# Kernel optimization log

Measured on AMD Instinct MI355X. Metric: run time of the kernel, lower is better.

Reference implementation:

```python
import jax, jax.numpy as jnp
import numpy as np

TINY = 1e-6

def _norm(x):
    return x / (jnp.linalg.norm(x, axis=-1, keepdims=True) + TINY)

def setup_inputs() -> dict:
    key = jax.random.key(0)
    ks = jax.random.split(key, 8)
    N, L, S, H = 8192, 128, 8, 16
    points = jax.random.normal(ks[0], (N, 3), dtype=jnp.float32)
    normals = _norm(jax.random.normal(ks[1], (N, 3), dtype=jnp.float32))
    # orthonormal root rotation (world -> canonical)
    root_rot, _ = jnp.linalg.qr(jax.random.normal(ks[2], (3, 3), dtype=jnp.float32))
    lgtSGLobes = jax.random.normal(ks[3], (L, 3), dtype=jnp.float32)
    # SG sharpness must be > 1 so arccos(1 - 1/lambda) is well defined
    lgtSGLambdas = jax.random.uniform(ks[4], (L, 1), dtype=jnp.float32) * 30.0 + 5.0
    r_theta_random = jax.random.uniform(ks[5], (N, L, S), dtype=jnp.float32)
    W1 = jax.random.normal(ks[6], (6, H), dtype=jnp.float32) * 0.5
    b1 = jnp.zeros((H,), dtype=jnp.float32)
    W2 = jax.random.normal(ks[7], (H, 1), dtype=jnp.float32) * 0.5
    b2 = jnp.zeros((1,), dtype=jnp.float32)
    return {"points": points, "normals": normals, "root_rot": root_rot,
            "lgtSGLobes": lgtSGLobes, "lgtSGLambdas": lgtSGLambdas,
            "r_theta_random": r_theta_random, "W1": W1, "b1": b1, "W2": W2, "b2": b2}

def reference(points, normals, root_rot, lgtSGLobes, lgtSGLambdas,
              r_theta_random, W1, b1, W2, b2):
    # points/normals: [N,3]; lgtSGLobes: [L,3]; r_theta_random: [N,L,S]
    N = points.shape[0]
    L, S = r_theta_random.shape[1], r_theta_random.shape[2]
    l = _norm(lgtSGLobes)                                  # [L,3] SG lobe axes
    z = jnp.zeros_like(l).at[:, 2].set(1.0)
    U = _norm(jnp.cross(z, l))                             # local frame around lobe
    V = _norm(jnp.cross(l, U))
    sharp = lgtSGLambdas[:, 0]                             # [L]
    r_phi = jnp.clip(jnp.arccos(1.0 - 1.0 / sharp), None, np.pi / 3.0)  # [L]
    lin = (jnp.arange(S, dtype=points.dtype) / S)          # stratified offsets
    r_theta = (r_theta_random / S + lin) * (2.0 * np.pi)   # [N,L,S]
    st, ct = jnp.sin(r_theta), jnp.cos(r_theta)            # [N,L,S]
    sp, cp = jnp.sin(r_phi), jnp.cos(r_phi)                # [L]
    # importance-sampled directions around each lobe: [N,L,S,3]
    sample_dir = (U[None, :, None, :] * (ct * sp[None, :, None])[..., None]
                  + V[None, :, None, :] * (st * sp[None, :, None])[..., None]
                  + l[None, :, None, :] * cp[None, :, None, None])
    # hemisphere mask (normals . sample_dir > eps)
    cos_term = jnp.einsum('nd,nlsd->nls', normals, sample_dir) > TINY
    # rotate query dirs to canonical frame: (-dir) @ root_rot
    input_dir = jnp.einsum('nlsd,de->nlse', -sample_dir, root_rot)
    # visibility MLP on (point, dir); concat avoided by splitting W1
    h = jax.nn.relu(jnp.einsum('nlsd,dh->nlsh', input_dir, W1[3:])
                    + (points @ W1[:3])[:, None, None, :] + b1)   # [N,L,S,H]
    pred_vis = jax.nn.sigmoid(jnp.einsum('nlsh,ho->nlso', h, W2)[..., 0] + b2[0])
    vis = jnp.where(cos_term, pred_vis, 0.0)               # masked scatter-back
    # SG weights exp(lambda*(dir.lobe - 1)); weighted reduction over samples
    w = jnp.exp(sharp[None, :, None] * (jnp.einsum('nlsd,ld->nls', sample_dir, l) - 1.0))
    return jnp.sum(vis * w, axis=-1) / (jnp.sum(w, axis=-1) + TINY)  # [N,L]
```

## Files before the change

kernel.cpp:

```cpp
#include <hip/hip_runtime.h>
#include <math.h>

typedef _Float16 h2 __attribute__((ext_vector_type(2)));
typedef __fp16  hh2 __attribute__((ext_vector_type(2)));

constexpr int Lc = 128;
constexpr int Sc = 8;

constexpr int F_OFF  = 3072;
constexpr int WQ_OFF = 4096;
constexpr int PB_OFF = 4224;
constexpr int LDS_DW = 4240;

static __device__ __forceinline__ h2 pk(float a, float b) {
    return __builtin_bit_cast(h2, __builtin_amdgcn_cvt_pkrtz(a, b));
}
static __device__ __forceinline__ h2 u2h(unsigned u) {
    return __builtin_bit_cast(h2, u);
}
static __device__ __forceinline__ unsigned h2u(h2 v) {
    return __builtin_bit_cast(unsigned, v);
}
static __device__ __forceinline__ float fdot2f(h2 a, h2 b, float c) {
#if __has_builtin(__builtin_amdgcn_fdot2)
    return __builtin_amdgcn_fdot2(__builtin_bit_cast(hh2, a),
                                  __builtin_bit_cast(hh2, b), c, false);
#else
    return c + (float)a.x * (float)b.x + (float)a.y * (float)b.y;
#endif
}
static __device__ __forceinline__ float fast_exp2(float x) {
#if __has_builtin(__builtin_amdgcn_exp2f)
    return __builtin_amdgcn_exp2f(x);
#else
    return exp2f(x);
#endif
}

__global__ __launch_bounds__(256, 4) void vis_fused(
    const float* __restrict__ points,
    const float* __restrict__ normals,
    const float* __restrict__ root_rot,
    const float* __restrict__ lobes,
    const float* __restrict__ lambdas,
    const float* __restrict__ rtheta,
    const float* __restrict__ W1,
    const float* __restrict__ b1,
    const float* __restrict__ W2,
    const float* __restrict__ b2,
    float* __restrict__ out, int N)
{
    __shared__ __align__(16) unsigned lds[LDS_DW];
    const int tid = threadIdx.x;
    const int li  = tid & (Lc - 1);

    {
        float lx = lobes[li*3+0], ly = lobes[li*3+1], lz = lobes[li*3+2];
        float inv = 1.0f / (sqrtf(lx*lx + ly*ly + lz*lz) + 1e-6f);
        lx *= inv; ly *= inv; lz *= inv;

        float ux = -ly, uy = lx;
        inv = 1.0f / (sqrtf(ux*ux + uy*uy) + 1e-6f);
        ux *= inv; uy *= inv;

        float vx = -lz*uy, vy = lz*ux, vz = lx*uy - ly*ux;
        inv = 1.0f / (sqrtf(vx*vx + vy*vy + vz*vz) + 1e-6f);
        vx *= inv; vy *= inv; vz *= inv;

        float sharp = lambdas[li];
        float cp = fmaxf(1.0f - 1.0f/sharp, 0.5f);
        float sp = sqrtf(fmaxf(1.0f - cp*cp, 0.0f));

        float uxs = ux*sp, uys = uy*sp;
        float vxs = vx*sp, vys = vy*sp, vzs = vz*sp;
        float lxc = lx*cp, lyc = ly*cp, lzc = lz*cp;

        const float r0 = root_rot[0], r1 = root_rot[1], r2 = root_rot[2];
        const float r3 = root_rot[3], r4 = root_rot[4], r5 = root_rot[5];
        const float r6 = root_rot[6], r7 = root_rot[7], r8 = root_rot[8];

        float Ur0 = -(uxs*r0 + uys*r3);
        float Ur1 = -(uxs*r1 + uys*r4);
        float Ur2 = -(uxs*r2 + uys*r5);
        float Vr0 = -(vxs*r0 + vys*r3 + vzs*r6);
        float Vr1 = -(vxs*r1 + vys*r4 + vzs*r7);
        float Vr2 = -(vxs*r2 + vys*r5 + vzs*r8);
        float Lr0 = -(lxc*r0 + lyc*r3 + lzc*r6);
        float Lr1 = -(lxc*r1 + lyc*r4 + lzc*r7);
        float Lr2 = -(lxc*r2 + lyc*r5 + lzc*r8);

        const int k0 = (tid < 128) ? 0 : 4;
        unsigned av[4], bv[4], dv[4];
        #pragma unroll
        for (int j = 0; j < 4; ++j) {
            int h0 = 2*(k0 + j), h1 = h0 + 1;
            float a0  = Ur0*W1[48+h0] + Ur1*W1[64+h0] + Ur2*W1[80+h0];
            float a1  = Ur0*W1[48+h1] + Ur1*W1[64+h1] + Ur2*W1[80+h1];
            float bb0 = Vr0*W1[48+h0] + Vr1*W1[64+h0] + Vr2*W1[80+h0];
            float bb1 = Vr0*W1[48+h1] + Vr1*W1[64+h1] + Vr2*W1[80+h1];
            float d0  = Lr0*W1[48+h0] + Lr1*W1[64+h0] + Lr2*W1[80+h0];
            float d1  = Lr0*W1[48+h1] + Lr1*W1[64+h1] + Lr2*W1[80+h1];
            av[j] = h2u(pk(a0, a1));
            bv[j] = h2u(pk(bb0, bb1));
            dv[j] = h2u(pk(d0, d1));
        }
        #pragma unroll
        for (int j = 0; j < 4; j += 2) {
            int g = (k0 + j) >> 1;
            *(uint2*)(lds + (0*4 + g)*256 + li*2) = (uint2){av[j], av[j+1]};
            *(uint2*)(lds + (1*4 + g)*256 + li*2) = (uint2){bv[j], bv[j+1]};
            *(uint2*)(lds + (2*4 + g)*256 + li*2) = (uint2){dv[j], dv[j+1]};
        }

        float* wf = (float*)lds;
        if (tid < 128) {
            *(float2*)(wf + F_OFF + 0*256 + li*2) = (float2){uxs, uys};
            *(float2*)(wf + F_OFF + 1*256 + li*2) = (float2){vxs, vys};
            *(float2*)(wf + F_OFF + 2*256 + li*2) = (float2){vzs, lxc};
            *(float2*)(wf + F_OFF + 3*256 + li*2) = (float2){lyc, lzc};
            float wq = __expf(sharp * (cp - 1.0f));
            wf[WQ_OFF + li] = wq / (8.0f * wq + 1e-6f);
        } else if (tid < 130) {
            int p = (blockIdx.x << 1) + (tid - 128);
            if (p < N) {
                float px = points[3*p], py = points[3*p+1], pz = points[3*p+2];
                #pragma unroll
                for (int k = 0; k < 8; ++k) {
                    int h0 = 2*k, h1 = 2*k + 1;
                    float v0 = b1[h0] + px*W1[h0] + py*W1[16+h0] + pz*W1[32+h0];
                    float v1 = b1[h1] + px*W1[h1] + py*W1[16+h1] + pz*W1[32+h1];
                    lds[PB_OFF + (tid - 128)*8 + k] = h2u(pk(v0, v1));
                }
            }
        }
    }
    __syncthreads();

    const int idx = blockIdx.x * 256 + tid;
    if (idx >= N * Lc) return;
    const int n = (blockIdx.x << 1) + (tid >> 7);

    uint2 t[12];
    #pragma unroll
    for (int g = 0; g < 12; ++g)
        t[g] = *(const uint2*)(lds + g*256 + li*2);
    const float* wf = (const float*)lds;
    float2 g0 = *(const float2*)(wf + F_OFF + 0*256 + li*2);
    float2 g1 = *(const float2*)(wf + F_OFF + 1*256 + li*2);
    float2 g2 = *(const float2*)(wf + F_OFF + 2*256 + li*2);
    float2 g3 = *(const float2*)(wf + F_OFF + 3*256 + li*2);
    float wqp = wf[WQ_OFF + li];

    const float4 q0 = *reinterpret_cast<const float4*>(rtheta + (size_t)idx * Sc);
    const float4 q1 = *reinterpret_cast<const float4*>(rtheta + (size_t)idx * Sc + 4);
    float rs[Sc] = {q0.x, q0.y, q0.z, q0.w, q1.x, q1.y, q1.z, q1.w};

    int nu = __builtin_amdgcn_readfirstlane(n);
    const float* nn = normals + 3*(size_t)nu;
    float nx = nn[0], ny = nn[1], nz = nn[2];
    const unsigned* pbp = lds + PB_OFF + (tid >> 7)*8;

    h2 A[8] = {u2h(t[0].x), u2h(t[0].y), u2h(t[1].x), u2h(t[1].y),
               u2h(t[2].x), u2h(t[2].y), u2h(t[3].x), u2h(t[3].y)};
    h2 B[8] = {u2h(t[4].x), u2h(t[4].y), u2h(t[5].x), u2h(t[5].y),
               u2h(t[6].x), u2h(t[6].y), u2h(t[7].x), u2h(t[7].y)};
    h2 G[8] = {u2h(pbp[0]) + u2h(t[8].x),  u2h(pbp[1]) + u2h(t[8].y),
               u2h(pbp[2]) + u2h(t[9].x),  u2h(pbp[3]) + u2h(t[9].y),
               u2h(pbp[4]) + u2h(t[10].x), u2h(pbp[5]) + u2h(t[10].y),
               u2h(pbp[6]) + u2h(t[11].x), u2h(pbp[7]) + u2h(t[11].y)};

    h2 W2h[8];
    #pragma unroll
    for (int k = 0; k < 8; ++k) W2h[k] = pk(W2[2*k], W2[2*k+1]);
    float b2c = -b2[0] * 1.44269504f;

    float nU = nx*g0.x + ny*g0.y;
    float nV = nx*g1.x + ny*g1.y + nz*g2.x;
    float nL = nx*g2.y + ny*g3.x + nz*g3.y;

    const h2 zero = {(_Float16)0.0f, (_Float16)0.0f};
    float svis = 0.0f;
    #pragma unroll
    for (int s = 0; s < Sc; ++s) {
        float f  = fmaf(rs[s], 0.125f, (float)s * 0.125f);
        float st = __builtin_amdgcn_sinf(f);
        float ct = __builtin_amdgcn_cosf(f);
        float ndot = fmaf(ct, nU, fmaf(st, nV, nL));

        h2 ct2 = pk(ct, ct);
        h2 st2 = pk(st, st);

        float acc = 0.0f;
        #pragma unroll
        for (int k = 0; k < 8; ++k) {
            h2 hv = __builtin_elementwise_fma(ct2, A[k],
                     __builtin_elementwise_fma(st2, B[k], G[k]));
            hv = __builtin_elementwise_max(hv, zero);
            acc = fdot2f(hv, W2h[k], acc);
        }
        float e = fast_exp2(fmaf(acc, -1.44269504f, b2c));
        float pred = __builtin_amdgcn_rcpf(1.0f + e);
        svis += (ndot > 1e-6f) ? pred : 0.0f;
    }

    out[idx] = svis * wqp;
}

extern "C" void kernel_launch(void* const* d_in, const int* in_sizes, int n_in,
                              void* d_out, int out_size, void* d_ws, size_t ws_size,
                              hipStream_t stream) {
    const float* points  = (const float*)d_in[0];
    const float* normals = (const float*)d_in[1];
    const float* root_rot= (const float*)d_in[2];
    const float* lobes   = (const float*)d_in[3];
    const float* lambdas = (const float*)d_in[4];
    const float* rtheta  = (const float*)d_in[5];
    const float* W1      = (const float*)d_in[6];
    const float* b1      = (const float*)d_in[7];
    const float* W2      = (const float*)d_in[8];
    const float* b2      = (const float*)d_in[9];
    float* out = (float*)d_out;
    (void)d_ws; (void)ws_size;

    int N = in_sizes[0] / 3;
    int total = N * Lc;
    vis_fused<<<(total + 255) / 256, 256, 0, stream>>>(
        points, normals, root_rot, lobes, lambdas, rtheta,
        W1, b1, W2, b2, out, N);
}
```

Before: 26.52 us.

## Process four tiles per block and drop LDS staging of lobe constants

Measured after the change: 26.26 us. About the same (-1.0%).

```diff
diff --git a/kernel.cpp b/kernel.cpp
--- a/kernel.cpp
+++ b/kernel.cpp
@@ -6,20 +6,10 @@
 
 constexpr int Lc = 128;
 constexpr int Sc = 8;
-
-constexpr int F_OFF  = 3072;
-constexpr int WQ_OFF = 4096;
-constexpr int PB_OFF = 4224;
-constexpr int LDS_DW = 4240;
+constexpr int TILES = 4;
 
 static __device__ __forceinline__ h2 pk(float a, float b) {
     return __builtin_bit_cast(h2, __builtin_amdgcn_cvt_pkrtz(a, b));
-}
-static __device__ __forceinline__ h2 u2h(unsigned u) {
-    return __builtin_bit_cast(h2, u);
-}
-static __device__ __forceinline__ unsigned h2u(h2 v) {
-    return __builtin_bit_cast(unsigned, v);
 }
 static __device__ __forceinline__ float fdot2f(h2 a, h2 b, float c) {
 #if __has_builtin(__builtin_amdgcn_fdot2)
@@ -37,7 +27,7 @@
 #endif
 }
 
-__global__ __launch_bounds__(256, 4) void vis_fused(
+__global__ __launch_bounds__(256, 4) void vis_all(
     const float* __restrict__ points,
     const float* __restrict__ normals,
     const float* __restrict__ root_rot,
@@ -50,10 +40,19 @@
     const float* __restrict__ b2,
     float* __restrict__ out, int N)
 {
-    __shared__ __align__(16) unsigned lds[LDS_DW];
-    const int tid = threadIdx.x;
-    const int li  = tid & (Lc - 1);
+    const int tid   = threadIdx.x;
+    const int li    = tid & (Lc - 1);
+    const int total = N * Lc;
+    const int base0 = blockIdx.x * (256 * TILES) + tid;
 
+    float4 p0 = {0,0,0,0}, p1 = {0,0,0,0};
+    if (base0 < total) {
+        p0 = *reinterpret_cast<const float4*>(rtheta + (size_t)base0 * Sc);
+        p1 = *reinterpret_cast<const float4*>(rtheta + (size_t)base0 * Sc + 4);
+    }
+
+    h2 A[8], B[8], D[8], W2h[8];
+    float uxs, uys, vxs, vys, vzs, lxc, lyc, lzc, wqp, b2c;
     {
         float lx = lobes[li*3+0], ly = lobes[li*3+1], lz = lobes[li*3+2];
         float inv = 1.0f / (sqrtf(lx*lx + ly*ly + lz*lz) + 1e-6f);
@@ -71,9 +70,9 @@
         float cp = fmaxf(1.0f - 1.0f/sharp, 0.5f);
         float sp = sqrtf(fmaxf(1.0f - cp*cp, 0.0f));
 
-        float uxs = ux*sp, uys = uy*sp;
-        float vxs = vx*sp, vys = vy*sp, vzs = vz*sp;
-        float lxc = lx*cp, lyc = ly*cp, lzc = lz*cp;
+        uxs = ux*sp; uys = uy*sp;
+        vxs = vx*sp; vys = vy*sp; vzs = vz*sp;
+        lxc = lx*cp; lyc = ly*cp; lzc = lz*cp;
 
         const float r0 = root_rot[0], r1 = root_rot[1], r2 = root_rot[2];
         const float r3 = root_rot[3], r4 = root_rot[4], r5 = root_rot[5];
@@ -89,121 +88,90 @@
         float Lr1 = -(lxc*r1 + lyc*r4 + lzc*r7);
         float Lr2 = -(lxc*r2 + lyc*r5 + lzc*r8);
 
-        const int k0 = (tid < 128) ? 0 : 4;
-        unsigned av[4], bv[4], dv[4];
         #pragma unroll
-        for (int j = 0; j < 4; ++j) {
-            int h0 = 2*(k0 + j), h1 = h0 + 1;
+        for (int k = 0; k < 8; ++k) {
+            int h0 = 2*k, h1 = 2*k + 1;
             float a0  = Ur0*W1[48+h0] + Ur1*W1[64+h0] + Ur2*W1[80+h0];
             float a1  = Ur0*W1[48+h1] + Ur1*W1[64+h1] + Ur2*W1[80+h1];
             float bb0 = Vr0*W1[48+h0] + Vr1*W1[64+h0] + Vr2*W1[80+h0];
             float bb1 = Vr0*W1[48+h1] + Vr1*W1[64+h1] + Vr2*W1[80+h1];
             float d0  = Lr0*W1[48+h0] + Lr1*W1[64+h0] + Lr2*W1[80+h0];
             float d1  = Lr0*W1[48+h1] + Lr1*W1[64+h1] + Lr2*W1[80+h1];
-            av[j] = h2u(pk(a0, a1));
-            bv[j] = h2u(pk(bb0, bb1));
-            dv[j] = h2u(pk(d0, d1));
+            A[k] = pk(a0, a1);
+            B[k] = pk(bb0, bb1);
+            D[k] = pk(d0, d1);
+            W2h[k] = pk(W2[h0], W2[h1]);
         }
+        float wq = __expf(sharp * (cp - 1.0f));
+        wqp = wq / (8.0f * wq + 1e-6f);
+        b2c = -b2[0] * 1.44269504f;
+    }
+
+    auto tile = [&](int t, float4 q0, float4 q1) {
+        const int idx = base0 + t * 256;
+        if (idx >= total) return;
+        const int n  = idx >> 7;
+        const int nu = __builtin_amdgcn_readfirstlane(n);
+
+        const float* nn = normals + 3*(size_t)nu;
+        float nx = nn[0], ny = nn[1], nz = nn[2];
+        const float* pp = points + 3*(size_t)nu;
+        float px = pp[0], py = pp[1], pz = pp[2];
+
+        h2 G[8];
         #pragma unroll
-        for (int j = 0; j < 4; j += 2) {
-            int g = (k0 + j) >> 1;
-            *(uint2*)(lds + (0*4 + g)*256 + li*2) = (uint2){av[j], av[j+1]};
-            *(uint2*)(lds + (1*4 + g)*256 + li*2) = (uint2){bv[j], bv[j+1]};
-            *(uint2*)(lds + (2*4 + g)*256 + li*2) = (uint2){dv[j], dv[j+1]};
+        for (int k = 0; k < 8; ++k) {
+            int h0 = 2*k, h1 = 2*k + 1;
+            float v0 = b1[h0] + px*W1[h0] + py*W1[16+h0] + pz*W1[32+h0];
+            float v1 = b1[h1] + px*W1[h1] + py*W1[16+h1] + pz*W1[32+h1];
+            G[k] = pk(v0, v1) + D[k];
         }
 
-        float* wf = (float*)lds;
-        if (tid < 128) {
-            *(float2*)(wf + F_OFF + 0*256 + li*2) = (float2){uxs, uys};
-            *(float2*)(wf + F_OFF + 1*256 + li*2) = (float2){vxs, vys};
-            *(float2*)(wf + F_OFF + 2*256 + li*2) = (float2){vzs, lxc};
-            *(float2*)(wf + F_OFF + 3*256 + li*2) = (float2){lyc, lzc};
-            float wq = __expf(sharp * (cp - 1.0f));
-            wf[WQ_OFF + li] = wq / (8.0f * wq + 1e-6f);
-        } else if (tid < 130) {
-            int p = (blockIdx.x << 1) + (tid - 128);
-            if (p < N) {
-                float px = points[3*p], py = points[3*p+1], pz = points[3*p+2];
-                #pragma unroll
-                for (int k = 0; k < 8; ++k) {
-                    int h0 = 2*k, h1 = 2*k + 1;
-                    float v0 = b1[h0] + px*W1[h0] + py*W1[16+h0] + pz*W1[32+h0];
-                    float v1 = b1[h1] + px*W1[h1] + py*W1[16+h1] + pz*W1[32+h1];
-                    lds[PB_OFF + (tid - 128)*8 + k] = h2u(pk(v0, v1));
-                }
+        float rs[Sc] = {q0.x, q0.y, q0.z, q0.w, q1.x, q1.y, q1.z, q1.w};
+
+        float nU = nx*uxs + ny*uys;
+        float nV = nx*vxs + ny*vys + nz*vzs;
+        float nL = nx*lxc + ny*lyc + nz*lzc;
+
+        const h2 zero = {(_Float16)0.0f, (_Float16)0.0f};
+        float svis = 0.0f;
+        #pragma unroll
+        for (int s = 0; s < Sc; ++s) {
+            float f  = fmaf(rs[s], 0.125f, (float)s * 0.125f);
+            float st = __builtin_amdgcn_sinf(f);
+            float ct = __builtin_amdgcn_cosf(f);
+            float ndot = fmaf(ct, nU, fmaf(st, nV, nL));
+
+            h2 ct2 = pk(ct, ct);
+            h2 st2 = pk(st, st);
+
+            float acc = 0.0f;
+            #pragma unroll
+            for (int k = 0; k < 8; ++k) {
+                h2 hv = __builtin_elementwise_fma(ct2, A[k],
+                         __builtin_elementwise_fma(st2, B[k], G[k]));
+                hv = __builtin_elementwise_max(hv, zero);
+                acc = fdot2f(hv, W2h[k], acc);
             }
+            float e = fast_exp2(fmaf(acc, -1.44269504f, b2c));
+            float pred = __builtin_amdgcn_rcpf(1.0f + e);
+            svis += (ndot > 1e-6f) ? pred : 0.0f;
         }
+
+        out[idx] = svis * wqp;
+    };
+
+    tile(0, p0, p1);
+    #pragma unroll 1
+    for (int t = 1; t < TILES; ++t) {
+        const int idx = base0 + t * 256;
+        float4 q0 = {0,0,0,0}, q1 = {0,0,0,0};
+        if (idx < total) {
+            q0 = *reinterpret_cast<const float4*>(rtheta + (size_t)idx * Sc);
+            q1 = *reinterpret_cast<const float4*>(rtheta + (size_t)idx * Sc + 4);
+        }
+        tile(t, q0, q1);
     }
-    __syncthreads();
-
-    const int idx = blockIdx.x * 256 + tid;
-    if (idx >= N * Lc) return;
-    const int n = (blockIdx.x << 1) + (tid >> 7);
-
-    uint2 t[12];
-    #pragma unroll
-    for (int g = 0; g < 12; ++g)
-        t[g] = *(const uint2*)(lds + g*256 + li*2);
-    const float* wf = (const float*)lds;
-    float2 g0 = *(const float2*)(wf + F_OFF + 0*256 + li*2);
-    float2 g1 = *(const float2*)(wf + F_OFF + 1*256 + li*2);
-    float2 g2 = *(const float2*)(wf + F_OFF + 2*256 + li*2);
-    float2 g3 = *(const float2*)(wf + F_OFF + 3*256 + li*2);
-    float wqp = wf[WQ_OFF + li];
-
-    const float4 q0 = *reinterpret_cast<const float4*>(rtheta + (size_t)idx * Sc);
-    const float4 q1 = *reinterpret_cast<const float4*>(rtheta + (size_t)idx * Sc + 4);
-    float rs[Sc] = {q0.x, q0.y, q0.z, q0.w, q1.x, q1.y, q1.z, q1.w};
-
-    int nu = __builtin_amdgcn_readfirstlane(n);
-    const float* nn = normals + 3*(size_t)nu;
-    float nx = nn[0], ny = nn[1], nz = nn[2];
-    const unsigned* pbp = lds + PB_OFF + (tid >> 7)*8;
-
-    h2 A[8] = {u2h(t[0].x), u2h(t[0].y), u2h(t[1].x), u2h(t[1].y),
-               u2h(t[2].x), u2h(t[2].y), u2h(t[3].x), u2h(t[3].y)};
-    h2 B[8] = {u2h(t[4].x), u2h(t[4].y), u2h(t[5].x), u2h(t[5].y),
-               u2h(t[6].x), u2h(t[6].y), u2h(t[7].x), u2h(t[7].y)};
-    h2 G[8] = {u2h(pbp[0]) + u2h(t[8].x),  u2h(pbp[1]) + u2h(t[8].y),
-               u2h(pbp[2]) + u2h(t[9].x),  u2h(pbp[3]) + u2h(t[9].y),
-               u2h(pbp[4]) + u2h(t[10].x), u2h(pbp[5]) + u2h(t[10].y),
-               u2h(pbp[6]) + u2h(t[11].x), u2h(pbp[7]) + u2h(t[11].y)};
-
-    h2 W2h[8];
-    #pragma unroll
-    for (int k = 0; k < 8; ++k) W2h[k] = pk(W2[2*k], W2[2*k+1]);
-    float b2c = -b2[0] * 1.44269504f;
-
-    float nU = nx*g0.x + ny*g0.y;
-    float nV = nx*g1.x + ny*g1.y + nz*g2.x;
-    float nL = nx*g2.y + ny*g3.x + nz*g3.y;
-
-    const h2 zero = {(_Float16)0.0f, (_Float16)0.0f};
-    float svis = 0.0f;
-    #pragma unroll
-    for (int s = 0; s < Sc; ++s) {
-        float f  = fmaf(rs[s], 0.125f, (float)s * 0.125f);
-        float st = __builtin_amdgcn_sinf(f);
-        float ct = __builtin_amdgcn_cosf(f);
-        float ndot = fmaf(ct, nU, fmaf(st, nV, nL));
-
-        h2 ct2 = pk(ct, ct);
-        h2 st2 = pk(st, st);
-
-        float acc = 0.0f;
-        #pragma unroll
-        for (int k = 0; k < 8; ++k) {
-            h2 hv = __builtin_elementwise_fma(ct2, A[k],
-                     __builtin_elementwise_fma(st2, B[k], G[k]));
-            hv = __builtin_elementwise_max(hv, zero);
-            acc = fdot2f(hv, W2h[k], acc);
-        }
-        float e = fast_exp2(fmaf(acc, -1.44269504f, b2c));
-        float pred = __builtin_amdgcn_rcpf(1.0f + e);
-        svis += (ndot > 1e-6f) ? pred : 0.0f;
-    }
-
-    out[idx] = svis * wqp;
 }
 
 extern "C" void kernel_launch(void* const* d_in, const int* in_sizes, int n_in,
@@ -224,7 +192,7 @@
 
     int N = in_sizes[0] / 3;
     int total = N * Lc;
-    vis_fused<<<(total + 255) / 256, 256, 0, stream>>>(
-        points, normals, root_rot, lobes, lambdas, rtheta,
-        W1, b1, W2, b2, out, N);
+    int blocks = (total + 256*TILES - 1) / (256*TILES);
+    vis_all<<<blocks, 256, 0, stream>>>(points, normals, root_rot, lobes,
+                                        lambdas, rtheta, W1, b1, W2, b2, out, N);
 }
```
